# Kernel tuning notes

Measured on AMD Instinct MI355X. Metric: run time of the kernel, lower is better.

## Reference

```python
import jax, jax.numpy as jnp
import numpy as np

N_NODES = 100000
N_EDGES = 3200000
NFEAT = 256
NHID = 256


def setup_inputs() -> dict:
    key = jax.random.key(0)
    k_x, k_ws, k_wn, k_src, k_dst = jax.random.split(key, 5)
    x = jax.random.normal(k_x, (N_NODES, NFEAT), dtype=jnp.float32)
    W_self = jax.random.normal(k_ws, (NFEAT, NHID), dtype=jnp.float32) * (1.0 / np.sqrt(NFEAT))
    W_neigh = jax.random.normal(k_wn, (NFEAT, NHID), dtype=jnp.float32) * (1.0 / np.sqrt(NFEAT))
    b = jnp.zeros((NHID,), dtype=jnp.float32)
    edge_src = jax.random.randint(k_src, (N_EDGES,), 0, N_NODES, dtype=jnp.int32)
    edge_dst = jax.random.randint(k_dst, (N_EDGES,), 0, N_NODES, dtype=jnp.int32)
    return {"x": x, "W_self": W_self, "W_neigh": W_neigh, "b": b,
            "edge_src": edge_src, "edge_dst": edge_dst}


def reference(x, W_self, W_neigh, b, edge_src, edge_dst):
    n = x.shape[0]
    # mean aggregation over incoming edges: gather src feats, scatter-add to dst
    msg = x[edge_src]                                              # [E, F]
    agg = jax.ops.segment_sum(msg, edge_dst, num_segments=n)       # [N, F]
    deg = jax.ops.segment_sum(jnp.ones_like(edge_dst, dtype=x.dtype),
                              edge_dst, num_segments=n)            # [N]
    h_neigh = agg / jnp.maximum(deg, 1.0)[:, None]                 # mean (0 for isolated)
    # SAGEConv 'mean': fc_self(x) + fc_neigh(h_neigh) (bias on neigh branch)
    out = x @ W_self + h_neigh @ W_neigh + b                       # [N, H]
    return jax.nn.relu(out)
```

## Files before the change

kernel.cpp:

```cpp
#include <hip/hip_runtime.h>
#include <stdint.h>

typedef __attribute__((ext_vector_type(8))) short bf16x8;
typedef __attribute__((ext_vector_type(4))) float f32x4;
typedef __attribute__((ext_vector_type(2))) float f32x2;

#define NF 256
#define NH 256
#define KTOT 512
#define BM 128
#define BN 128
#define BK2 64
#define LDP2 72
#define EB 256
#define NBIN 512

static __device__ __forceinline__ unsigned short f2bf(float f){
  union { float f; unsigned int u; } v; v.f = f;
  unsigned int r = v.u + 0x7fffu + ((v.u >> 16) & 1u);
  return (unsigned short)(r >> 16);
}
static __device__ __forceinline__ unsigned int f2e4(float f){
  union { float f; unsigned int u; } v; v.f = f;
  unsigned int s = v.u >> 31;
  unsigned int mag = v.u & 0x7fffffffu;
  if (mag > 0x43E00000u) mag = 0x43E00000u;
  unsigned int r = mag + 0x7ffffu + ((mag >> 20) & 1u);
  if (r < 0x3C800000u) return 0u;
  return (s << 7) | (((r >> 20) - 960u) & 0x7fu);
}

__global__ void k_cvt_xq(const float* __restrict__ x, unsigned int* __restrict__ xq, int n8){
  for (int i = blockIdx.x*blockDim.x + threadIdx.x; i < n8; i += gridDim.x*blockDim.x){
    const float4* p = (const float4*)(x + (size_t)i*8);
    float4 a = p[0], b = p[1];
    unsigned int w0 = f2e4(a.x) | (f2e4(a.y)<<8) | (f2e4(a.z)<<16) | (f2e4(a.w)<<24);
    unsigned int w1 = f2e4(b.x) | (f2e4(b.y)<<8) | (f2e4(b.z)<<16) | (f2e4(b.w)<<24);
    uint2 o; o.x = w0; o.y = w1;
    ((uint2*)xq)[i] = o;
  }
}

__global__ void k_cvt_w(const float* __restrict__ Ws, const float* __restrict__ Wn,
                        unsigned short* __restrict__ Wt){
  int t = blockIdx.x*blockDim.x + threadIdx.x;
  if (t >= NH*KTOT) return;
  int n = t >> 9, k = t & 511;
  float v = (k < NF) ? Ws[(size_t)k*NH + n] : Wn[(size_t)(k-NF)*NH + n];
  Wt[t] = (unsigned short)f2bf(v);
}

__global__ void __launch_bounds__(256) k_bhist(const int* __restrict__ dst,
                                               int* __restrict__ H, int ne){
  __shared__ int lh[NBIN];
  int blk = blockIdx.x, t = threadIdx.x;
  for (int i = t; i < NBIN; i += 256) lh[i] = 0;
  __syncthreads();
  int chunk = (ne + EB - 1) / EB;
  int e0 = blk * chunk, e1 = ne < e0 + chunk ? ne : e0 + chunk;
  for (int e = e0 + t; e < e1; e += 256)
    atomicAdd(&lh[((unsigned)dst[e]) >> 8], 1);
  __syncthreads();
  for (int i = t; i < NBIN; i += 256) H[i*EB + blk] = lh[i];
}

__global__ void k_partial(const int* __restrict__ deg, int* __restrict__ partial, int n){
  __shared__ int sm[256];
  int b = blockIdx.x, t = threadIdx.x;
  int i0 = b*1024 + t*4;
  int s = 0;
  if (i0 + 3 < n){ int4 v = *(const int4*)(deg + i0); s = v.x+v.y+v.z+v.w; }
  else { for (int j=0;j<4;j++) if (i0+j < n) s += deg[i0+j]; }
  sm[t] = s; __syncthreads();
  for (int d = 128; d > 0; d >>= 1){ if (t < d) sm[t] += sm[t+d]; __syncthreads(); }
  if (t == 0) partial[b] = sm[0];
}

__global__ void k_scanp(int* __restrict__ partial, int nb){
  __shared__ int sm[128];
  int t = threadIdx.x;
  int v = (t < nb) ? partial[t] : 0;
  sm[t] = v; __syncthreads();
  for (int d = 1; d < 128; d <<= 1){
    int u = (t >= d) ? sm[t-d] : 0; __syncthreads();
    sm[t] += u; __syncthreads();
  }
  if (t < nb) partial[t] = sm[t] - v;
}

__global__ void k_scanapply(const int* __restrict__ deg, const int* __restrict__ partial,
                            int* __restrict__ off, int n, int ne){
  __shared__ int sm[256];
  int b = blockIdx.x, t = threadIdx.x;
  int i0 = b*1024 + t*4;
  int d0=0,d1=0,d2=0,d3=0;
  if (i0 + 3 < n){ int4 v = *(const int4*)(deg + i0); d0=v.x; d1=v.y; d2=v.z; d3=v.w; }
  else { if(i0<n)d0=deg[i0]; if(i0+1<n)d1=deg[i0+1]; if(i0+2<n)d2=deg[i0+2]; if(i0+3<n)d3=deg[i0+3]; }
  int s = d0+d1+d2+d3;
  sm[t] = s; __syncthreads();
  for (int d = 1; d < 256; d <<= 1){
    int u = (t >= d) ? sm[t-d] : 0; __syncthreads();
    sm[t] += u; __syncthreads();
  }
  int run = partial[b] + sm[t] - s;
  if (i0   < n) off[i0]   = run; run += d0;
  if (i0+1 < n) off[i0+1] = run; run += d1;
  if (i0+2 < n) off[i0+2] = run; run += d2;
  if (i0+3 < n) off[i0+3] = run;
  if (b == 0 && t == 0) off[n] = ne;
}

__global__ void __launch_bounds__(256) k_bscat(const int* __restrict__ src,
                                               const int* __restrict__ dst,
                                               const int* __restrict__ base,
                                               unsigned int* __restrict__ bkt, int ne){
  __shared__ int lc[NBIN];
  __shared__ int lb[NBIN];
  int blk = blockIdx.x, t = threadIdx.x;
  for (int i = t; i < NBIN; i += 256){ lc[i] = 0; lb[i] = base[i*EB + blk]; }
  __syncthreads();
  int chunk = (ne + EB - 1) / EB;
  int e0 = blk * chunk, e1 = ne < e0 + chunk ? ne : e0 + chunk;
  for (int e = e0 + t; e < e1; e += 256){
    int d = dst[e];
    int bin = ((unsigned)d) >> 8;
    int p = lb[bin] + atomicAdd(&lc[bin], 1);
    bkt[p] = (((unsigned)src[e]) << 8) | ((unsigned)d & 255u);
  }
}

__global__ void __launch_bounds__(256) k_csr(const unsigned int* __restrict__ bkt,
                                             const int* __restrict__ base,
                                             int* __restrict__ off, int* __restrict__ col,
                                             int nn, int ne){
  __shared__ int lh[256], sc[256], se[256], lc[256];
  int b = blockIdx.x, t = threadIdx.x;
  int n0 = base[b*EB], n1 = base[(b+1)*EB];
  lh[t] = 0; lc[t] = 0;
  __syncthreads();
  for (int e = n0 + t; e < n1; e += 256)
    atomicAdd(&lh[bkt[e] & 255u], 1);
  __syncthreads();
  int v = lh[t];
  sc[t] = v; __syncthreads();
  for (int d = 1; d < 256; d <<= 1){
    int u = (t >= d) ? sc[t-d] : 0; __syncthreads();
    sc[t] += u; __syncthreads();
  }
  int excl = sc[t] - v;
  se[t] = excl;
  int node = b*256 + t;
  if (node <= nn) off[node] = n0 + excl;
  __syncthreads();
  for (int e = n0 + t; e < n1; e += 256){
    unsigned u = bkt[e];
    int low = (int)(u & 255u);
    int r = atomicAdd(&lc[low], 1);
    col[n0 + se[low] + r] = (int)(u >> 8);
  }
}

static __device__ __forceinline__ void acc4(unsigned int v, float& a0, float& a1, float& a2, float& a3){
#if __has_builtin(__builtin_amdgcn_cvt_pk_f32_fp8)
  f32x2 lo = __builtin_amdgcn_cvt_pk_f32_fp8((int)v, false);
  f32x2 hi = __builtin_amdgcn_cvt_pk_f32_fp8((int)v, true);
  a0 += lo[0]; a1 += lo[1]; a2 += hi[0]; a3 += hi[1];
#else
  #pragma unroll
  for (int j = 0; j < 4; j++){
    unsigned int b = (v >> (8*j)) & 0xffu;
    unsigned int tt = b & 0x7fu;
    union { unsigned int u; float f; } w;
    w.u = ((tt + 960u) << 20) | ((b & 0x80u) << 24);
    float f = tt ? w.f : 0.f;
    if (j==0) a0 += f; else if (j==1) a1 += f; else if (j==2) a2 += f; else a3 += f;
  }
#endif
}
static __device__ __forceinline__ ushort4 dec8(unsigned int v){
#if __has_builtin(__builtin_amdgcn_cvt_pk_f32_fp8)
  f32x2 lo = __builtin_amdgcn_cvt_pk_f32_fp8((int)v, false);
  f32x2 hi = __builtin_amdgcn_cvt_pk_f32_fp8((int)v, true);
  ushort4 o; o.x=f2bf(lo[0]); o.y=f2bf(lo[1]); o.z=f2bf(hi[0]); o.w=f2bf(hi[1]);
  return o;
#else
  ushort4 o; unsigned short r[4];
  #pragma unroll
  for (int j = 0; j < 4; j++){
    unsigned int b = (v >> (8*j)) & 0xffu;
    unsigned int tt = b & 0x7fu;
    union { unsigned int u; float f; } w;
    w.u = ((tt + 960u) << 20) | ((b & 0x80u) << 24);
    r[j] = tt ? f2bf(w.f) : (unsigned short)0;
  }
  o.x=r[0]; o.y=r[1]; o.z=r[2]; o.w=r[3];
  return o;
#endif
}

__global__ void __launch_bounds__(256) k_agg(const unsigned int* __restrict__ xw,
                                             const int* __restrict__ off,
                                             const int* __restrict__ col,
                                             unsigned int* __restrict__ hq, int n){
  int w = threadIdx.x >> 6;
  int lane = threadIdx.x & 63;
  int node = blockIdx.x*4 + w;
  if (node >= n) return;
  int e0 = off[node], e1 = off[node+1];
  int deg = e1 - e0;
  float a0=0.f, a1=0.f, a2=0.f, a3=0.f;
  for (int c0 = 0; c0 < deg; c0 += 64){
    int len = deg - c0; if (len > 64) len = 64;
    int cv = 0;
    if (lane < len) cv = col[e0 + c0 + lane];
    int i = 0;
    for (; i + 8 <= len; i += 8){
      int s0 = __builtin_amdgcn_readlane(cv, i+0);
      int s1 = __builtin_amdgcn_readlane(cv, i+1);
      int s2 = __builtin_amdgcn_readlane(cv, i+2);
      int s3 = __builtin_amdgcn_readlane(cv, i+3);
      int s4 = __builtin_amdgcn_readlane(cv, i+4);
      int s5 = __builtin_amdgcn_readlane(cv, i+5);
      int s6 = __builtin_amdgcn_readlane(cv, i+6);
      int s7 = __builtin_amdgcn_readlane(cv, i+7);
      unsigned int u0 = xw[(size_t)s0*64 + lane];
      unsigned int u1 = xw[(size_t)s1*64 + lane];
      unsigned int u2 = xw[(size_t)s2*64 + lane];
      unsigned int u3 = xw[(size_t)s3*64 + lane];
      unsigned int u4 = xw[(size_t)s4*64 + lane];
      unsigned int u5 = xw[(size_t)s5*64 + lane];
      unsigned int u6 = xw[(size_t)s6*64 + lane];
      unsigned int u7 = xw[(size_t)s7*64 + lane];
      acc4(u0,a0,a1,a2,a3); acc4(u1,a0,a1,a2,a3);
      acc4(u2,a0,a1,a2,a3); acc4(u3,a0,a1,a2,a3);
      acc4(u4,a0,a1,a2,a3); acc4(u5,a0,a1,a2,a3);
      acc4(u6,a0,a1,a2,a3); acc4(u7,a0,a1,a2,a3);
    }
    for (; i < len; ++i){
      int s = __builtin_amdgcn_readlane(cv, i);
      unsigned int u = xw[(size_t)s*64 + lane];
      acc4(u,a0,a1,a2,a3);
    }
  }
  float inv = 1.f / (float)(deg > 1 ? deg : 1);
  unsigned int o = f2e4(a0*inv) | (f2e4(a1*inv)<<8) | (f2e4(a2*inv)<<16) | (f2e4(a3*inv)<<24);
  hq[(size_t)node*64 + lane] = o;
}

__global__ void __launch_bounds__(256) k_gemm(const float* __restrict__ xf,
                                              const unsigned char* __restrict__ hq,
                                              const unsigned short* __restrict__ Wt,
                                              const float* __restrict__ bias,
                                              float* __restrict__ out, int M){
  __shared__ unsigned short As[BM*LDP2];
  __shared__ unsigned short Bs[BN*LDP2];
  int t = threadIdx.x;
  int m0 = blockIdx.x * BM;
  int n0 = blockIdx.y * BN;
  int w = t >> 6, lane = t & 63;
  int wm = w >> 1, wn = w & 1;
  int lrow = lane & 15, k8 = (lane >> 4) * 8;

  f32x4 acc[4][4];
  #pragma unroll
  for (int i=0;i<4;i++)
    #pragma unroll
    for (int j=0;j<4;j++) acc[i][j] = (f32x4){0.f,0.f,0.f,0.f};

  for (int kk = 0; kk < KTOT; kk += BK2){
    __syncthreads();
    if (kk < NF){
      #pragma unroll
      for (int q = 0; q < 4; q++){
        int chunk = q*256 + t;
        int r = chunk >> 3, c8 = (chunk & 7) * 8;
        int gr = m0 + r; if (gr > M-1) gr = M-1;
        const float* src = xf + (size_t)gr*NF + kk + c8;
        float4 u0 = ((const float4*)src)[0];
        float4 u1 = ((const float4*)src)[1];
        ushort4 o0, o1;
        o0.x=f2bf(u0.x); o0.y=f2bf(u0.y); o0.z=f2bf(u0.z); o0.w=f2bf(u0.w);
        o1.x=f2bf(u1.x); o1.y=f2bf(u1.y); o1.z=f2bf(u1.z); o1.w=f2bf(u1.w);
        *(ushort4*)(&As[r*LDP2 + c8])     = o0;
        *(ushort4*)(&As[r*LDP2 + c8 + 4]) = o1;
      }
    } else {
      #pragma unroll
      for (int q = 0; q < 4; q++){
        int chunk = q*256 + t;
        int r = chunk >> 3, c8 = (chunk & 7) * 8;
        int gr = m0 + r; if (gr > M-1) gr = M-1;
        uint2 v = *(const uint2*)(hq + (size_t)gr*NF + (kk - NF) + c8);
        *(ushort4*)(&As[r*LDP2 + c8])     = dec8(v.x);
        *(ushort4*)(&As[r*LDP2 + c8 + 4]) = dec8(v.y);
      }
    }
    #pragma unroll
    for (int q = 0; q < 4; q++){
      int chunk = q*256 + t;
      int r = chunk >> 3, c8 = (chunk & 7) * 8;
      int4 v = *(const int4*)(Wt + (size_t)(n0 + r)*KTOT + kk + c8);
      *(int4*)(&Bs[r*LDP2 + c8]) = v;
    }
    __syncthreads();
    #pragma unroll
    for (int ks = 0; ks < 2; ks++){
      bf16x8 af[4], bfr[4];
      #pragma unroll
      for (int mi=0;mi<4;mi++)
        af[mi] = *(const bf16x8*)(&As[(wm*64 + mi*16 + lrow)*LDP2 + ks*32 + k8]);
      #pragma unroll
      for (int ni=0;ni<4;ni++)
        bfr[ni] = *(const bf16x8*)(&Bs[(wn*64 + ni*16 + lrow)*LDP2 + ks*32 + k8]);
      #pragma unroll
      for (int mi=0;mi<4;mi++)
        #pragma unroll
        for (int ni=0;ni<4;ni++)
          acc[mi][ni] = __builtin_amdgcn_mfma_f32_16x16x32_bf16(af[mi], bfr[ni], acc[mi][ni], 0, 0, 0);
    }
  }

  #pragma unroll
  for (int ni=0;ni<4;ni++){
    int cn = n0 + wn*64 + ni*16 + lrow;
    float bv = bias[cn];
    #pragma unroll
    for (int mi=0;mi<4;mi++){
      #pragma unroll
      for (int r=0;r<4;r++){
        int rm = m0 + wm*64 + mi*16 + (lane>>4)*4 + r;
        if (rm < M){
          float v = acc[mi][ni][r] + bv;
          out[(size_t)rm*NH + cn] = v > 0.f ? v : 0.f;
        }
      }
    }
  }
}

extern "C" void kernel_launch(void* const* d_in, const int* in_sizes, int n_in,
                              void* d_out, int out_size, void* d_ws, size_t ws_size,
                              hipStream_t stream){
  const float* x      = (const float*)d_in[0];
  const float* Wself  = (const float*)d_in[1];
  const float* Wneigh = (const float*)d_in[2];
  const float* bias   = (const float*)d_in[3];
  const int*   esrc   = (const int*)d_in[4];
  const int*   edst   = (const int*)d_in[5];
  const int nn = in_sizes[0] / NF;
  const int ne = in_sizes[4];

  char* w = (char*)d_ws;
  auto alloc = [&](size_t bytes)->char*{
    char* p = w; w += (bytes + 511) & ~size_t(511); return p;
  };
  unsigned char*  xq  = (unsigned char*)alloc((size_t)nn*NF);
  unsigned char*  hq  = (unsigned char*)alloc((size_t)nn*NF);
  unsigned int* bkt   = (unsigned int*)alloc((size_t)ne*4);
  int* col            = (int*)alloc((size_t)ne*4);
  int* H              = (int*)alloc((size_t)(NBIN*EB + 1)*4);
  int* base           = (int*)alloc((size_t)(NBIN*EB + 1)*4);
  int* off            = (int*)alloc((size_t)(nn+1)*4);
  unsigned short* Wt  = (unsigned short*)alloc((size_t)NH*KTOT*2);
  int* partial        = (int*)alloc(4096);

  const int nH = NBIN*EB;
  const int nb = nH / 1024;

  k_cvt_xq<<<2048, 256, 0, stream>>>(x, (unsigned int*)xq, nn*NF/8);
  k_cvt_w<<<(NH*KTOT + 255)/256, 256, 0, stream>>>(Wself, Wneigh, Wt);
  k_bhist<<<EB, 256, 0, stream>>>(edst, H, ne);
  k_partial<<<nb, 256, 0, stream>>>(H, partial, nH);
  k_scanp<<<1, 128, 0, stream>>>(partial, nb);
  k_scanapply<<<nb, 256, 0, stream>>>(H, partial, base, nH, ne);
  k_bscat<<<EB, 256, 0, stream>>>(esrc, edst, base, bkt, ne);
  k_csr<<<NBIN, 256, 0, stream>>>(bkt, base, off, col, nn, ne);
  k_agg<<<(nn + 3)/4, 256, 0, stream>>>((const unsigned int*)xq, off, col, (unsigned int*)hq, nn);
  dim3 gg((nn + BM - 1)/BM, NH/BN);
  k_gemm<<<gg, 256, 0, stream>>>(x, hq, Wt, bias, (float*)d_out, nn);
}
```

Before: 340.8 us.

## Pre-convert x to bf16 and load GEMM tiles directly to LDS with swizzle

The conversion kernel now also writes a bf16 copy of x. The GEMM then streams the x and weight tiles straight into LDS with global_load_lds, using an XOR-swizzled 128-byte row layout in place of the padded layout, and the fp8 aggregate tiles use the same swizzle. This removes the per-tile fp32-to-bf16 conversion and the register round trip from the GEMM, at the cost of an extra bf16 buffer written in the prepass. The bucket buffer is also reused as the aggregate buffer, and the edge-block count for the histogram and scatter is halved.

```diff
diff --git a/kernel.cpp b/kernel.cpp
--- a/kernel.cpp
+++ b/kernel.cpp
@@ -10,9 +10,8 @@
 #define KTOT 512
 #define BM 128
 #define BN 128
-#define BK2 64
-#define LDP2 72
-#define EB 256
+#define BK 64
+#define EB 128
 #define NBIN 512
 
 static __device__ __forceinline__ unsigned short f2bf(float f){
@@ -29,137 +28,6 @@
   if (r < 0x3C800000u) return 0u;
   return (s << 7) | (((r >> 20) - 960u) & 0x7fu);
 }
-
-__global__ void k_cvt_xq(const float* __restrict__ x, unsigned int* __restrict__ xq, int n8){
-  for (int i = blockIdx.x*blockDim.x + threadIdx.x; i < n8; i += gridDim.x*blockDim.x){
-    const float4* p = (const float4*)(x + (size_t)i*8);
-    float4 a = p[0], b = p[1];
-    unsigned int w0 = f2e4(a.x) | (f2e4(a.y)<<8) | (f2e4(a.z)<<16) | (f2e4(a.w)<<24);
-    unsigned int w1 = f2e4(b.x) | (f2e4(b.y)<<8) | (f2e4(b.z)<<16) | (f2e4(b.w)<<24);
-    uint2 o; o.x = w0; o.y = w1;
-    ((uint2*)xq)[i] = o;
-  }
-}
-
-__global__ void k_cvt_w(const float* __restrict__ Ws, const float* __restrict__ Wn,
-                        unsigned short* __restrict__ Wt){
-  int t = blockIdx.x*blockDim.x + threadIdx.x;
-  if (t >= NH*KTOT) return;
-  int n = t >> 9, k = t & 511;
-  float v = (k < NF) ? Ws[(size_t)k*NH + n] : Wn[(size_t)(k-NF)*NH + n];
-  Wt[t] = (unsigned short)f2bf(v);
-}
-
-__global__ void __launch_bounds__(256) k_bhist(const int* __restrict__ dst,
-                                               int* __restrict__ H, int ne){
-  __shared__ int lh[NBIN];
-  int blk = blockIdx.x, t = threadIdx.x;
-  for (int i = t; i < NBIN; i += 256) lh[i] = 0;
-  __syncthreads();
-  int chunk = (ne + EB - 1) / EB;
-  int e0 = blk * chunk, e1 = ne < e0 + chunk ? ne : e0 + chunk;
-  for (int e = e0 + t; e < e1; e += 256)
-    atomicAdd(&lh[((unsigned)dst[e]) >> 8], 1);
-  __syncthreads();
-  for (int i = t; i < NBIN; i += 256) H[i*EB + blk] = lh[i];
-}
-
-__global__ void k_partial(const int* __restrict__ deg, int* __restrict__ partial, int n){
-  __shared__ int sm[256];
-  int b = blockIdx.x, t = threadIdx.x;
-  int i0 = b*1024 + t*4;
-  int s = 0;
-  if (i0 + 3 < n){ int4 v = *(const int4*)(deg + i0); s = v.x+v.y+v.z+v.w; }
-  else { for (int j=0;j<4;j++) if (i0+j < n) s += deg[i0+j]; }
-  sm[t] = s; __syncthreads();
-  for (int d = 128; d > 0; d >>= 1){ if (t < d) sm[t] += sm[t+d]; __syncthreads(); }
-  if (t == 0) partial[b] = sm[0];
-}
-
-__global__ void k_scanp(int* __restrict__ partial, int nb){
-  __shared__ int sm[128];
-  int t = threadIdx.x;
-  int v = (t < nb) ? partial[t] : 0;
-  sm[t] = v; __syncthreads();
-  for (int d = 1; d < 128; d <<= 1){
-    int u = (t >= d) ? sm[t-d] : 0; __syncthreads();
-    sm[t] += u; __syncthreads();
-  }
-  if (t < nb) partial[t] = sm[t] - v;
-}
-
-__global__ void k_scanapply(const int* __restrict__ deg, const int* __restrict__ partial,
-                            int* __restrict__ off, int n, int ne){
-  __shared__ int sm[256];
-  int b = blockIdx.x, t = threadIdx.x;
-  int i0 = b*1024 + t*4;
-  int d0=0,d1=0,d2=0,d3=0;
-  if (i0 + 3 < n){ int4 v = *(const int4*)(deg + i0); d0=v.x; d1=v.y; d2=v.z; d3=v.w; }
-  else { if(i0<n)d0=deg[i0]; if(i0+1<n)d1=deg[i0+1]; if(i0+2<n)d2=deg[i0+2]; if(i0+3<n)d3=deg[i0+3]; }
-  int s = d0+d1+d2+d3;
-  sm[t] = s; __syncthreads();
-  for (int d = 1; d < 256; d <<= 1){
-    int u = (t >= d) ? sm[t-d] : 0; __syncthreads();
-    sm[t] += u; __syncthreads();
-  }
-  int run = partial[b] + sm[t] - s;
-  if (i0   < n) off[i0]   = run; run += d0;
-  if (i0+1 < n) off[i0+1] = run; run += d1;
-  if (i0+2 < n) off[i0+2] = run; run += d2;
-  if (i0+3 < n) off[i0+3] = run;
-  if (b == 0 && t == 0) off[n] = ne;
-}
-
-__global__ void __launch_bounds__(256) k_bscat(const int* __restrict__ src,
-                                               const int* __restrict__ dst,
-                                               const int* __restrict__ base,
-                                               unsigned int* __restrict__ bkt, int ne){
-  __shared__ int lc[NBIN];
-  __shared__ int lb[NBIN];
-  int blk = blockIdx.x, t = threadIdx.x;
-  for (int i = t; i < NBIN; i += 256){ lc[i] = 0; lb[i] = base[i*EB + blk]; }
-  __syncthreads();
-  int chunk = (ne + EB - 1) / EB;
-  int e0 = blk * chunk, e1 = ne < e0 + chunk ? ne : e0 + chunk;
-  for (int e = e0 + t; e < e1; e += 256){
-    int d = dst[e];
-    int bin = ((unsigned)d) >> 8;
-    int p = lb[bin] + atomicAdd(&lc[bin], 1);
-    bkt[p] = (((unsigned)src[e]) << 8) | ((unsigned)d & 255u);
-  }
-}
-
-__global__ void __launch_bounds__(256) k_csr(const unsigned int* __restrict__ bkt,
-                                             const int* __restrict__ base,
-                                             int* __restrict__ off, int* __restrict__ col,
-                                             int nn, int ne){
-  __shared__ int lh[256], sc[256], se[256], lc[256];
-  int b = blockIdx.x, t = threadIdx.x;
-  int n0 = base[b*EB], n1 = base[(b+1)*EB];
-  lh[t] = 0; lc[t] = 0;
-  __syncthreads();
-  for (int e = n0 + t; e < n1; e += 256)
-    atomicAdd(&lh[bkt[e] & 255u], 1);
-  __syncthreads();
-  int v = lh[t];
-  sc[t] = v; __syncthreads();
-  for (int d = 1; d < 256; d <<= 1){
-    int u = (t >= d) ? sc[t-d] : 0; __syncthreads();
-    sc[t] += u; __syncthreads();
-  }
-  int excl = sc[t] - v;
-  se[t] = excl;
-  int node = b*256 + t;
-  if (node <= nn) off[node] = n0 + excl;
-  __syncthreads();
-  for (int e = n0 + t; e < n1; e += 256){
-    unsigned u = bkt[e];
-    int low = (int)(u & 255u);
-    int r = atomicAdd(&lc[low], 1);
-    col[n0 + se[low] + r] = (int)(u >> 8);
-  }
-}
-
 static __device__ __forceinline__ void acc4(unsigned int v, float& a0, float& a1, float& a2, float& a3){
 #if __has_builtin(__builtin_amdgcn_cvt_pk_f32_fp8)
   f32x2 lo = __builtin_amdgcn_cvt_pk_f32_fp8((int)v, false);
@@ -196,6 +64,152 @@
   o.x=r[0]; o.y=r[1]; o.z=r[2]; o.w=r[3];
   return o;
 #endif
+}
+static __device__ __forceinline__ void gload16(const void* g, void* lds_wave_base, int lane){
+#if __has_builtin(__builtin_amdgcn_global_load_lds)
+  __builtin_amdgcn_global_load_lds(
+      (const __attribute__((address_space(1))) unsigned int*)g,
+      (__attribute__((address_space(3))) unsigned int*)lds_wave_base, 16, 0, 0);
+  (void)lane;
+#else
+  *(int4*)((char*)lds_wave_base + (size_t)lane*16) = *(const int4*)g;
+#endif
+}
+
+__global__ void k_cvt_x(const float* __restrict__ x, unsigned short* __restrict__ xb,
+                        unsigned int* __restrict__ xq, int n8){
+  for (int i = blockIdx.x*blockDim.x + threadIdx.x; i < n8; i += gridDim.x*blockDim.x){
+    const float4* p = (const float4*)(x + (size_t)i*8);
+    float4 a = p[0], b = p[1];
+    ushort4 o0, o1;
+    o0.x=f2bf(a.x); o0.y=f2bf(a.y); o0.z=f2bf(a.z); o0.w=f2bf(a.w);
+    o1.x=f2bf(b.x); o1.y=f2bf(b.y); o1.z=f2bf(b.z); o1.w=f2bf(b.w);
+    ushort4* q = (ushort4*)(xb + (size_t)i*8);
+    q[0] = o0; q[1] = o1;
+    unsigned int w0 = f2e4(a.x) | (f2e4(a.y)<<8) | (f2e4(a.z)<<16) | (f2e4(a.w)<<24);
+    unsigned int w1 = f2e4(b.x) | (f2e4(b.y)<<8) | (f2e4(b.z)<<16) | (f2e4(b.w)<<24);
+    uint2 o; o.x = w0; o.y = w1;
+    ((uint2*)xq)[i] = o;
+  }
+}
+
+__global__ void k_cvt_w(const float* __restrict__ Ws, const float* __restrict__ Wn,
+                        unsigned short* __restrict__ Wt){
+  int t = blockIdx.x*blockDim.x + threadIdx.x;
+  if (t >= NH*KTOT) return;
+  int n = t >> 9, k = t & 511;
+  float v = (k < NF) ? Ws[(size_t)k*NH + n] : Wn[(size_t)(k-NF)*NH + n];
+  Wt[t] = (unsigned short)f2bf(v);
+}
+
+__global__ void __launch_bounds__(256) k_bhist(const int* __restrict__ dst,
+                                               int* __restrict__ H, int ne){
+  __shared__ int lh[NBIN];
+  int blk = blockIdx.x, t = threadIdx.x;
+  for (int i = t; i < NBIN; i += 256) lh[i] = 0;
+  __syncthreads();
+  int chunk = (ne + EB - 1) / EB;
+  int e0 = blk * chunk, e1 = ne < e0 + chunk ? ne : e0 + chunk;
+  for (int e = e0 + t; e < e1; e += 256)
+    atomicAdd(&lh[((unsigned)dst[e]) >> 8], 1);
+  __syncthreads();
+  for (int i = t; i < NBIN; i += 256) H[i*EB + blk] = lh[i];
+}
+
+__global__ void k_partial(const int* __restrict__ deg, int* __restrict__ partial, int n){
+  __shared__ int sm[256];
+  int b = blockIdx.x, t = threadIdx.x;
+  int i0 = b*1024 + t*4;
+  int s = 0;
+  if (i0 + 3 < n){ int4 v = *(const int4*)(deg + i0); s = v.x+v.y+v.z+v.w; }
+  else { for (int j=0;j<4;j++) if (i0+j < n) s += deg[i0+j]; }
+  sm[t] = s; __syncthreads();
+  for (int d = 128; d > 0; d >>= 1){ if (t < d) sm[t] += sm[t+d]; __syncthreads(); }
+  if (t == 0) partial[b] = sm[0];
+}
+
+__global__ void k_scanp(int* __restrict__ partial, int nb){
+  __shared__ int sm[128];
+  int t = threadIdx.x;
+  int v = (t < nb) ? partial[t] : 0;
+  sm[t] = v; __syncthreads();
+  for (int d = 1; d < 128; d <<= 1){
+    int u = (t >= d) ? sm[t-d] : 0; __syncthreads();
+    sm[t] += u; __syncthreads();
+  }
+  if (t < nb) partial[t] = sm[t] - v;
+}
+
+__global__ void k_scanapply(const int* __restrict__ deg, const int* __restrict__ partial,
+                            int* __restrict__ off, int n, int ne){
+  __shared__ int sm[256];
+  int b = blockIdx.x, t = threadIdx.x;
+  int i0 = b*1024 + t*4;
+  int d0=0,d1=0,d2=0,d3=0;
+  if (i0 + 3 < n){ int4 v = *(const int4*)(deg + i0); d0=v.x; d1=v.y; d2=v.z; d3=v.w; }
+  else { if(i0<n)d0=deg[i0]; if(i0+1<n)d1=deg[i0+1]; if(i0+2<n)d2=deg[i0+2]; if(i0+3<n)d3=deg[i0+3]; }
+  int s = d0+d1+d2+d3;
+  sm[t] = s; __syncthreads();
+  for (int d = 1; d < 256; d <<= 1){
+    int u = (t >= d) ? sm[t-d] : 0; __syncthreads();
+    sm[t] += u; __syncthreads();
+  }
+  int run = partial[b] + sm[t] - s;
+  if (i0   < n) off[i0]   = run; run += d0;
+  if (i0+1 < n) off[i0+1] = run; run += d1;
+  if (i0+2 < n) off[i0+2] = run; run += d2;
+  if (i0+3 < n) off[i0+3] = run;
+  if (b == 0 && t == 0) off[n] = ne;
+}
+
+__global__ void __launch_bounds__(256) k_bscat(const int* __restrict__ src,
+                                               const int* __restrict__ dst,
+                                               const int* __restrict__ base,
+                                               unsigned int* __restrict__ bkt, int ne){
+  __shared__ int lc[NBIN];
+  __shared__ int lb[NBIN];
+  int blk = blockIdx.x, t = threadIdx.x;
+  for (int i = t; i < NBIN; i += 256){ lc[i] = 0; lb[i] = base[i*EB + blk]; }
+  __syncthreads();
+  int chunk = (ne + EB - 1) / EB;
+  int e0 = blk * chunk, e1 = ne < e0 + chunk ? ne : e0 + chunk;
+  for (int e = e0 + t; e < e1; e += 256){
+    int d = dst[e];
+    int bin = ((unsigned)d) >> 8;
+    int p = lb[bin] + atomicAdd(&lc[bin], 1);
+    bkt[p] = (((unsigned)src[e]) << 8) | ((unsigned)d & 255u);
+  }
+}
+
+__global__ void __launch_bounds__(256) k_csr(const unsigned int* __restrict__ bkt,
+                                             const int* __restrict__ base,
+                                             int* __restrict__ off, int* __restrict__ col,
+                                             int nn, int ne){
+  __shared__ int lh[256], sc[256], se[256], lc[256];
+  int b = blockIdx.x, t = threadIdx.x;
+  int n0 = base[b*EB], n1 = base[(b+1)*EB];
+  lh[t] = 0; lc[t] = 0;
+  __syncthreads();
+  for (int e = n0 + t; e < n1; e += 256)
+    atomicAdd(&lh[bkt[e] & 255u], 1);
+  __syncthreads();
+  int v = lh[t];
+  sc[t] = v; __syncthreads();
+  for (int d = 1; d < 256; d <<= 1){
+    int u = (t >= d) ? sc[t-d] : 0; __syncthreads();
+    sc[t] += u; __syncthreads();
+  }
+  int excl = sc[t] - v;
+  se[t] = excl;
+  int node = b*256 + t;
+  if (node <= nn) off[node] = n0 + excl;
+  __syncthreads();
+  for (int e = n0 + t; e < n1; e += 256){
+    unsigned u = bkt[e];
+    int low = (int)(u & 255u);
+    int r = atomicAdd(&lc[low], 1);
+    col[n0 + se[low] + r] = (int)(u >> 8);
+  }
 }
 
 __global__ void __launch_bounds__(256) k_agg(const unsigned int* __restrict__ xw,
@@ -247,19 +261,22 @@
   hq[(size_t)node*64 + lane] = o;
 }
 
-__global__ void __launch_bounds__(256) k_gemm(const float* __restrict__ xf,
-                                              const unsigned char* __restrict__ hq,
+__global__ void __launch_bounds__(256) k_gemm(const unsigned short* __restrict__ xb,
+                                              const unsigned char*  __restrict__ hq,
                                               const unsigned short* __restrict__ Wt,
                                               const float* __restrict__ bias,
                                               float* __restrict__ out, int M){
-  __shared__ unsigned short As[BM*LDP2];
-  __shared__ unsigned short Bs[BN*LDP2];
+  __shared__ __align__(16) unsigned short As[BM*BK];
+  __shared__ __align__(16) unsigned short Bs[BN*BK];
   int t = threadIdx.x;
   int m0 = blockIdx.x * BM;
   int n0 = blockIdx.y * BN;
   int w = t >> 6, lane = t & 63;
   int wm = w >> 1, wn = w & 1;
-  int lrow = lane & 15, k8 = (lane >> 4) * 8;
+  int lrow = lane & 15;
+  int cgrp = (lane >> 4) * 16;
+  int row_s = t >> 3;
+  int slot  = t & 7;
 
   f32x4 acc[4][4];
   #pragma unroll
@@ -267,51 +284,53 @@
     #pragma unroll
     for (int j=0;j<4;j++) acc[i][j] = (f32x4){0.f,0.f,0.f,0.f};
 
-  for (int kk = 0; kk < KTOT; kk += BK2){
+  for (int kk = 0; kk < KTOT; kk += BK){
     __syncthreads();
     if (kk < NF){
       #pragma unroll
-      for (int q = 0; q < 4; q++){
-        int chunk = q*256 + t;
-        int r = chunk >> 3, c8 = (chunk & 7) * 8;
-        int gr = m0 + r; if (gr > M-1) gr = M-1;
-        const float* src = xf + (size_t)gr*NF + kk + c8;
-        float4 u0 = ((const float4*)src)[0];
-        float4 u1 = ((const float4*)src)[1];
-        ushort4 o0, o1;
-        o0.x=f2bf(u0.x); o0.y=f2bf(u0.y); o0.z=f2bf(u0.z); o0.w=f2bf(u0.w);
-        o1.x=f2bf(u1.x); o1.y=f2bf(u1.y); o1.z=f2bf(u1.z); o1.w=f2bf(u1.w);
-        *(ushort4*)(&As[r*LDP2 + c8])     = o0;
-        *(ushort4*)(&As[r*LDP2 + c8 + 4]) = o1;
+      for (int r = 0; r < 4; r++){
+        int row = r*32 + row_s;
+        const char* g = (const char*)(xb + (size_t)(m0 + row)*NF + kk)
+                        + ((slot ^ (row & 7)) << 4);
+        gload16(g, (char*)As + (size_t)(r*256 + (t & ~63))*16, lane);
       }
     } else {
       #pragma unroll
-      for (int q = 0; q < 4; q++){
-        int chunk = q*256 + t;
-        int r = chunk >> 3, c8 = (chunk & 7) * 8;
-        int gr = m0 + r; if (gr > M-1) gr = M-1;
-        uint2 v = *(const uint2*)(hq + (size_t)gr*NF + (kk - NF) + c8);
-        *(ushort4*)(&As[r*LDP2 + c8])     = dec8(v.x);
-        *(ushort4*)(&As[r*LDP2 + c8 + 4]) = dec8(v.y);
+      for (int r = 0; r < 4; r++){
+        int row = r*32 + row_s;
+        const unsigned char* g = hq + (size_t)(m0 + row)*NF + (kk - NF)
+                                 + ((slot ^ (row & 7)) << 3);
+        uint2 v = *(const uint2*)g;
+        ushort4 lo = dec8(v.x), hi = dec8(v.y);
+        char* dstb = (char*)As + (size_t)row*128 + slot*16;
+        *(ushort4*)dstb = lo;
+        *(ushort4*)(dstb + 8) = hi;
       }
     }
     #pragma unroll
-    for (int q = 0; q < 4; q++){
-      int chunk = q*256 + t;
-      int r = chunk >> 3, c8 = (chunk & 7) * 8;
-      int4 v = *(const int4*)(Wt + (size_t)(n0 + r)*KTOT + kk + c8);
-      *(int4*)(&Bs[r*LDP2 + c8]) = v;
+    for (int r = 0; r < 4; r++){
+      int row = r*32 + row_s;
+      const char* g = (const char*)(Wt + (size_t)(n0 + row)*KTOT + kk)
+                      + ((slot ^ (row & 7)) << 4);
+      gload16(g, (char*)Bs + (size_t)(r*256 + (t & ~63))*16, lane);
     }
     __syncthreads();
+
     #pragma unroll
     for (int ks = 0; ks < 2; ks++){
       bf16x8 af[4], bfr[4];
       #pragma unroll
-      for (int mi=0;mi<4;mi++)
-        af[mi] = *(const bf16x8*)(&As[(wm*64 + mi*16 + lrow)*LDP2 + ks*32 + k8]);
-      #pragma unroll
-      for (int ni=0;ni<4;ni++)
-        bfr[ni] = *(const bf16x8*)(&Bs[(wn*64 + ni*16 + lrow)*LDP2 + ks*32 + k8]);
+      for (int mi=0;mi<4;mi++){
+        int row = wm*64 + mi*16 + lrow;
+        int cb = (ks*64 + cgrp) ^ ((row & 7) << 4);
+        af[mi] = *(const bf16x8*)((const char*)As + (size_t)row*128 + cb);
+      }
+      #pragma unroll
+      for (int ni=0;ni<4;ni++){
+        int row = wn*64 + ni*16 + lrow;
+        int cb = (ks*64 + cgrp) ^ ((row & 7) << 4);
+        bfr[ni] = *(const bf16x8*)((const char*)Bs + (size_t)row*128 + cb);
+      }
       #pragma unroll
       for (int mi=0;mi<4;mi++)
         #pragma unroll
@@ -349,25 +368,28 @@
   const int*   edst   = (const int*)d_in[5];
   const int nn = in_sizes[0] / NF;
   const int ne = in_sizes[4];
+  const int mpad = ((nn + BM - 1) / BM) * BM;
 
   char* w = (char*)d_ws;
   auto alloc = [&](size_t bytes)->char*{
     char* p = w; w += (bytes + 511) & ~size_t(511); return p;
   };
+  unsigned short* xb  = (unsigned short*)alloc((size_t)mpad*NF*2);
   unsigned char*  xq  = (unsigned char*)alloc((size_t)nn*NF);
-  unsigned char*  hq  = (unsigned char*)alloc((size_t)nn*NF);
-  unsigned int* bkt   = (unsigned int*)alloc((size_t)ne*4);
+  char* hq_bkt        = alloc((size_t)mpad*NF);
   int* col            = (int*)alloc((size_t)ne*4);
-  int* H              = (int*)alloc((size_t)(NBIN*EB + 1)*4);
-  int* base           = (int*)alloc((size_t)(NBIN*EB + 1)*4);
+  int* H              = (int*)alloc((size_t)NBIN*EB*4);
+  int* base           = (int*)alloc(((size_t)NBIN*EB + 1)*4);
   int* off            = (int*)alloc((size_t)(nn+1)*4);
   unsigned short* Wt  = (unsigned short*)alloc((size_t)NH*KTOT*2);
   int* partial        = (int*)alloc(4096);
+  unsigned int* bkt   = (unsigned int*)hq_bkt;
+  unsigned char* hq   = (unsigned char*)hq_bkt;
 
   const int nH = NBIN*EB;
   const int nb = nH / 1024;
 
-  k_cvt_xq<<<2048, 256, 0, stream>>>(x, (unsigned int*)xq, nn*NF/8);
+  k_cvt_x<<<2048, 256, 0, stream>>>(x, xb, (unsigned int*)xq, nn*NF/8);
   k_cvt_w<<<(NH*KTOT + 255)/256, 256, 0, stream>>>(Wself, Wneigh, Wt);
   k_bhist<<<EB, 256, 0, stream>>>(edst, H, ne);
   k_partial<<<nb, 256, 0, stream>>>(H, partial, nH);
@@ -376,6 +398,6 @@
   k_bscat<<<EB, 256, 0, stream>>>(esrc, edst, base, bkt, ne);
   k_csr<<<NBIN, 256, 0, stream>>>(bkt, base, off, col, nn, ne);
   k_agg<<<(nn + 3)/4, 256, 0, stream>>>((const unsigned int*)xq, off, col, (unsigned int*)hq, nn);
-  dim3 gg((nn + BM - 1)/BM, NH/BN);
-  k_gemm<<<gg, 256, 0, stream>>>(x, hq, Wt, bias, (float*)d_out, nn);
-}
+  dim3 gg(mpad/BM, NH/BN);
+  k_gemm<<<gg, 256, 0, stream>>>(xb, hq, Wt, bias, (float*)d_out, nn);
+}
```

After: 381.3 us. 1.12x slower.
